# Kernel tuning notes

Hardware: AMD Instinct MI355X
Metric: run time of the kernel (lower is better)

The kernel has to match this reference:

```python
import jax, jax.numpy as jnp
import numpy as np

B, T, D, F, E, K = 4, 2048, 1024, 2048, 8, 2


def setup_inputs() -> dict:
    key = jax.random.key(0)
    ks = jax.random.split(key, 5)
    s = lambda n: 1.0 / np.sqrt(n)
    return {
        "x": jax.random.normal(ks[0], (B, T, D), jnp.float32),
        "gate_w": jax.random.normal(ks[1], (D, E), jnp.float32) * s(D),
        "gate_b": jnp.zeros((E,), jnp.float32),
        "w1": jax.random.normal(ks[2], (E, D, F), jnp.float32) * s(D),
        "b1": jnp.zeros((E, F), jnp.float32),
        "w2": jax.random.normal(ks[3], (E, F, D), jnp.float32) * s(F),
        "b2": jnp.zeros((E, D), jnp.float32),
    }


def reference(x, gate_w, gate_b, w1, b1, w2, b2):
    # Router: gate logits -> top-k -> softmax over the k selected logits
    logits = x @ gate_w + gate_b                      # [B,T,E]
    top_v, top_i = jax.lax.top_k(logits, K)           # [B,T,K]
    top_w = jax.nn.softmax(top_v, axis=-1)            # [B,T,K]
    # Dense combine weights per expert: w_full[b,t,e] = sum_k top_w * 1[top_i==e]
    one_hot = jax.nn.one_hot(top_i, E, dtype=x.dtype)  # [B,T,K,E]
    w_full = jnp.sum(top_w[..., None] * one_hot, axis=-2)  # [B,T,E]
    # All-experts FFN (batched over expert dim), exact-erf GELU as in nn.GELU()
    h = jax.nn.gelu(jnp.einsum('btd,edf->ebtf', x, w1) + b1[:, None, None, :],
                    approximate=False)                 # [E,B,T,F]
    y = jnp.einsum('ebtf,efd->ebtd', h, w2) + b2[:, None, None, :]  # [E,B,T,D]
    # Weighted combine (zero weight for unselected experts == masked dispatch)
    return jnp.einsum('bte,ebtd->btd', w_full, y)      # [B,T,D]
```

## Files before the change

kernel.cpp:

```cpp
#include <hip/hip_runtime.h>
#include <hip/hip_bf16.h>
#include <math.h>

#define B_ 4
#define T_ 2048
#define D_ 1024
#define F_ 2048
#define E_ 8
#define NT (B_ * T_)
#define NS (NT * 2)
#define CAP (NS + E_ * 256)

typedef __attribute__((ext_vector_type(8))) short short8;
typedef __attribute__((ext_vector_type(4))) float floatx4;

static __device__ __forceinline__ unsigned short f2bf(float f) {
  union { float f; unsigned u; } a; a.f = f;
  unsigned r = a.u + 0x7fffu + ((a.u >> 16) & 1u);
  return (unsigned short)(r >> 16);
}

static __device__ __forceinline__ float bf2f(unsigned u) {
  union { unsigned u; float f; } a; a.u = u << 16; return a.f;
}

static __device__ __forceinline__ void gld16(const unsigned short* g, unsigned short* l) {
  __builtin_amdgcn_global_load_lds(
      (const __attribute__((address_space(1))) void*)g,
      (__attribute__((address_space(3))) void*)l, 16, 0, 0);
}

static __device__ __forceinline__ float gelu_f(float v) {
  float ax = fabsf(v) * 0.70710678118654752f;
  float t = __builtin_amdgcn_rcpf(1.f + 0.3275911f * ax);
  float e = __builtin_amdgcn_exp2f(-ax * ax * 1.44269504088896f);
  float p = t * (0.254829592f +
            t * (-0.284496736f +
            t * (1.421413741f +
            t * (-1.453152027f +
            t * 1.061405429f))));
  float er = 1.f - p * e;
  er = copysignf(er, v);
  return 0.5f * v * (1.f + er);
}

__global__ void transpose_cvt(const float* __restrict__ in, unsigned short* __restrict__ out,
                              int R, int C) {
  __shared__ float tile[32][33];
  int e = blockIdx.z;
  const float* inp = in + (size_t)e * R * C;
  unsigned short* outp = out + (size_t)e * R * C;
  int c0 = blockIdx.x * 32, r0 = blockIdx.y * 32;
  int tx = threadIdx.x, ty = threadIdx.y;
#pragma unroll
  for (int j = 0; j < 4; j++)
    tile[ty + 8 * j][tx] = inp[(size_t)(r0 + ty + 8 * j) * C + c0 + tx];
  __syncthreads();
#pragma unroll
  for (int j = 0; j < 4; j++)
    outp[(size_t)(c0 + ty + 8 * j) * R + r0 + tx] = f2bf(tile[tx][ty + 8 * j]);
}

__global__ void router_k(const float* __restrict__ x, const float* __restrict__ gw,
                         const float* __restrict__ gb, int* __restrict__ ti,
                         float* __restrict__ tw) {
  int wid = threadIdx.x >> 6, lane = threadIdx.x & 63;
  int t = blockIdx.x * 4 + wid;
  const float* xr = x + (size_t)t * D_;
  float acc[E_];
#pragma unroll
  for (int e = 0; e < E_; e++) acc[e] = 0.f;
#pragma unroll
  for (int it = 0; it < D_ / 64; it++) {
    int d = it * 64 + lane;
    float xv = xr[d];
    const float* g = gw + d * E_;
#pragma unroll
    for (int e = 0; e < E_; e++) acc[e] += xv * g[e];
  }
#pragma unroll
  for (int off = 32; off > 0; off >>= 1)
#pragma unroll
    for (int e = 0; e < E_; e++) acc[e] += __shfl_xor(acc[e], off);
  if (lane == 0) {
    float v[E_];
#pragma unroll
    for (int e = 0; e < E_; e++) v[e] = acc[e] + gb[e];
    int i0 = 0; float v0 = v[0];
#pragma unroll
    for (int e = 1; e < E_; e++) if (v[e] > v0) { v0 = v[e]; i0 = e; }
    int i1 = -1; float v1 = -3.4e38f;
#pragma unroll
    for (int e = 0; e < E_; e++) if (e != i0 && v[e] > v1) { v1 = v[e]; i1 = e; }
    float ex = expf(v1 - v0);
    float w0 = 1.f / (1.f + ex);
    float w1 = ex / (1.f + ex);
    ti[2 * t] = i0; tw[2 * t] = w0;
    ti[2 * t + 1] = i1; tw[2 * t + 1] = w1;
  }
}

__global__ void count_prefix_k(const int* __restrict__ ti, int* __restrict__ offs,
                               int* __restrict__ cursors) {
  __shared__ int scnt[4][E_];
  int tid = threadIdx.x;
  int cnt[E_];
#pragma unroll
  for (int k = 0; k < E_; k++) cnt[k] = 0;
  for (int i = tid; i < NS; i += 256) {
    int e = ti[i];
#pragma unroll
    for (int k = 0; k < E_; k++) cnt[k] += (e == k) ? 1 : 0;
  }
#pragma unroll
  for (int off = 32; off > 0; off >>= 1)
#pragma unroll
    for (int k = 0; k < E_; k++) cnt[k] += __shfl_xor(cnt[k], off);
  int wid = tid >> 6, lane = tid & 63;
  if (lane == 0)
#pragma unroll
    for (int k = 0; k < E_; k++) scnt[wid][k] = cnt[k];
  __syncthreads();
  if (tid == 0) {
    int o = 0;
    for (int k = 0; k < E_; k++) {
      int c = scnt[0][k] + scnt[1][k] + scnt[2][k] + scnt[3][k];
      offs[k] = o;
      cursors[k] = o;
      o += (c + 255) & ~255;
    }
    offs[E_] = o;
  }
}

__global__ void fill_k(int* __restrict__ idx) {
  int s = blockIdx.x * 256 + threadIdx.x;
  if (s < CAP) idx[s] = 0;
}

__global__ void scatter_k(const int* __restrict__ ti, const float* __restrict__ tw,
                          int* __restrict__ cursors, int* __restrict__ idx,
                          int* __restrict__ pos_of) {
  int a = blockIdx.x * 256 + threadIdx.x;
  int lane = threadIdx.x & 63;
  int e = ti[a];
  unsigned long long m[E_];
#pragma unroll
  for (int k = 0; k < E_; k++) m[k] = __ballot(e == k);
  int base = 0;
  if (lane < E_) base = atomicAdd(&cursors[lane], __popcll(m[lane]));
  int myBase = __shfl(base, e);
  unsigned long long m_mine = 0;
#pragma unroll
  for (int k = 0; k < E_; k++) if (e == k) m_mine = m[k];
  int rank = __popcll(m_mine & ((1ull << lane) - 1ull));
  int pos = myBase + rank;
  idx[pos] = a >> 1;
  pos_of[a] = pos;
}

__global__ void gather_k(const float* __restrict__ x, const int* __restrict__ idx,
                         unsigned short* __restrict__ Xg) {
  int s = blockIdx.x;
  int t = idx[s];
  const float4* xr = (const float4*)(x + (size_t)t * D_);
  float4 v = xr[threadIdx.x];
  uint2 p;
  p.x = (unsigned)f2bf(v.x) | ((unsigned)f2bf(v.y) << 16);
  p.y = (unsigned)f2bf(v.z) | ((unsigned)f2bf(v.w) << 16);
  ((uint2*)(Xg + (size_t)s * D_))[threadIdx.x] = p;
}

template <int K, int N, bool GELU>
__global__ __launch_bounds__(512, 2) void gemm_k(const unsigned short* __restrict__ A,
                                                 const unsigned short* __restrict__ W,
                                                 const float* __restrict__ bias_all,
                                                 unsigned short* __restrict__ O,
                                                 const int* __restrict__ offs) {
  int slot0 = blockIdx.y * 256;
  if (slot0 >= offs[E_]) return;
  int e = 0;
  while (slot0 >= offs[e + 1]) e++;
  const unsigned short* Bp = W + (size_t)e * N * K;
  int n0 = blockIdx.x * 256;

  __shared__ unsigned short lA[2][256 * 64];
  __shared__ unsigned short lB[2][256 * 64];

  int tid = threadIdx.x;
  int wid = tid >> 6, lane = tid & 63;
  int wr = wid >> 2, wc = wid & 3;
  int quad = lane >> 4, l15 = lane & 15;
  int l7 = l15 & 7;

  int sr = lane >> 3;
  int ch = (lane & 7) ^ sr;
  const unsigned short* gA = A + (size_t)(slot0 + 8 * wid + sr) * K + ch * 8;
  const unsigned short* gB = Bp + (size_t)(n0 + 8 * wid + sr) * K + ch * 8;

#define STAGE_A(buf, q, kk) gld16(gA + (size_t)(q) * 64 * K + (size_t)(kk), \
                                  &lA[buf][((q) * 64 + 8 * wid) * 64])
#define STAGE_B(buf, q, kk) gld16(gB + (size_t)(q) * 64 * K + (size_t)(kk), \
                                  &lB[buf][((q) * 64 + 8 * wid) * 64])
#define SYNCV(n) asm volatile("s_waitcnt vmcnt(" #n ")\n\ts_barrier" ::: "memory")

#define PH(buf, mh, ks, ...) do {                                                   \
    short8 af_[4], bf_[4];                                                          \
    _Pragma("unroll")                                                               \
    for (int m_ = 0; m_ < 4; m_++) {                                                \
      int row_ = 128 * wr + 64 * (mh) + 16 * m_ + l15;                              \
      af_[m_] = *(const short8*)&lA[buf][row_ * 64 + ((((ks) << 2) | quad) ^ l7) * 8]; \
    }                                                                               \
    _Pragma("unroll")                                                               \
    for (int n_ = 0; n_ < 4; n_++) {                                                \
      int row_ = 64 * wc + 16 * n_ + l15;                                           \
      bf_[n_] = *(const short8*)&lB[buf][row_ * 64 + ((((ks) << 2) | quad) ^ l7) * 8]; \
    }                                                                               \
    __VA_ARGS__                                                                     \
    __builtin_amdgcn_sched_barrier(0x38F);                                          \
    __builtin_amdgcn_s_setprio(1);                                                  \
    _Pragma("unroll")                                                               \
    for (int m_ = 0; m_ < 4; m_++) {                                                \
      _Pragma("unroll")                                                             \
      for (int n_ = 0; n_ < 4; n_++)                                                \
        acc[4 * (mh) + m_][n_] = __builtin_amdgcn_mfma_f32_16x16x32_bf16(           \
            af_[m_], bf_[n_], acc[4 * (mh) + m_][n_], 0, 0, 0);                     \
    }                                                                               \
    __builtin_amdgcn_s_setprio(0);                                                  \
  } while (0)

  floatx4 acc[8][4];
#pragma unroll
  for (int mi = 0; mi < 8; mi++)
#pragma unroll
    for (int ni = 0; ni < 4; ni++) acc[mi][ni] = (floatx4){0.f, 0.f, 0.f, 0.f};

  STAGE_A(0, 0, 0); STAGE_A(0, 2, 0);
  STAGE_B(0, 0, 0); STAGE_B(0, 1, 0);
  STAGE_B(0, 2, 0); STAGE_B(0, 3, 0);
  __builtin_amdgcn_sched_barrier(0x38F);
  STAGE_A(0, 1, 0); STAGE_A(0, 3, 0);

  constexpr int NI = K / 128;
  for (int i = 0; i < NI; i++) {
    int kO = (2 * i + 1) * 64;
    int kE = (i + 1 < NI) ? (2 * i + 2) * 64 : 0;
    SYNCV(2);
    PH(0, 0, 0, STAGE_A(1, 0, kO); STAGE_A(1, 2, kO););
    PH(0, 0, 1, STAGE_B(1, 0, kO); STAGE_B(1, 1, kO););
    SYNCV(4);
    PH(0, 1, 0, STAGE_B(1, 2, kO); STAGE_B(1, 3, kO););
    PH(0, 1, 1, STAGE_A(1, 1, kO); STAGE_A(1, 3, kO););
    SYNCV(2);
    PH(1, 0, 0, STAGE_A(0, 0, kE); STAGE_A(0, 2, kE););
    PH(1, 0, 1, STAGE_B(0, 0, kE); STAGE_B(0, 1, kE););
    SYNCV(4);
    PH(1, 1, 0, STAGE_B(0, 2, kE); STAGE_B(0, 3, kE););
    PH(1, 1, 1, STAGE_A(0, 1, kE); STAGE_A(0, 3, kE););
  }

  const float* bias = bias_all + (size_t)e * N;
#pragma unroll
  for (int mi = 0; mi < 8; mi++) {
    int row = slot0 + 128 * wr + 16 * mi + quad * 4;
#pragma unroll
    for (int ni = 0; ni < 4; ni++) {
      int col = n0 + 64 * wc + 16 * ni + l15;
      float bv = bias[col];
#pragma unroll
      for (int r = 0; r < 4; r++) {
        float v = acc[mi][ni][r] + bv;
        if (GELU) v = gelu_f(v);
        O[(size_t)(row + r) * N + col] = f2bf(v);
      }
    }
  }
#undef STAGE_A
#undef STAGE_B
#undef SYNCV
#undef PH
}

__global__ void combine_k(const unsigned short* __restrict__ Yg,
                          const int* __restrict__ pos_of,
                          const float* __restrict__ tw, float* __restrict__ out) {
  int t = blockIdx.x;
  int p0 = pos_of[2 * t], p1 = pos_of[2 * t + 1];
  float w0 = tw[2 * t], w1 = tw[2 * t + 1];
  uint2 a = ((const uint2*)(Yg + (size_t)p0 * D_))[threadIdx.x];
  uint2 b = ((const uint2*)(Yg + (size_t)p1 * D_))[threadIdx.x];
  float4 r;
  r.x = w0 * bf2f(a.x & 0xffffu) + w1 * bf2f(b.x & 0xffffu);
  r.y = w0 * bf2f(a.x >> 16)     + w1 * bf2f(b.x >> 16);
  r.z = w0 * bf2f(a.y & 0xffffu) + w1 * bf2f(b.y & 0xffffu);
  r.w = w0 * bf2f(a.y >> 16)     + w1 * bf2f(b.y >> 16);
  ((float4*)(out + (size_t)t * D_))[threadIdx.x] = r;
}

extern "C" void kernel_launch(void* const* d_in, const int* in_sizes, int n_in,
                              void* d_out, int out_size, void* d_ws, size_t ws_size,
                              hipStream_t stream) {
  const float* x  = (const float*)d_in[0];
  const float* gw = (const float*)d_in[1];
  const float* gb = (const float*)d_in[2];
  const float* w1 = (const float*)d_in[3];
  const float* b1 = (const float*)d_in[4];
  const float* w2 = (const float*)d_in[5];
  const float* b2 = (const float*)d_in[6];
  float* out = (float*)d_out;

  char* p = (char*)d_ws;
  unsigned short* w1t = (unsigned short*)p; p += (size_t)E_ * D_ * F_ * 2;
  unsigned short* w2t = (unsigned short*)p; p += (size_t)E_ * D_ * F_ * 2;
  unsigned short* Xg  = (unsigned short*)p; p += (size_t)CAP * D_ * 2;
  unsigned short* H   = (unsigned short*)p; p += (size_t)CAP * F_ * 2;
  int*   idx    = (int*)p; p += (size_t)CAP * 4;
  int*   pos_of = (int*)p; p += (size_t)NS * 4;
  int*   ti     = (int*)p; p += (size_t)NS * 4;
  float* tw     = (float*)p; p += (size_t)NS * 4;
  int* cursors = (int*)p; p += 64;
  int* offs    = (int*)p; p += 64;
  unsigned short* Yg = Xg;

  dim3 tb(32, 8);
  transpose_cvt<<<dim3(F_ / 32, D_ / 32, E_), tb, 0, stream>>>(w1, w1t, D_, F_);
  transpose_cvt<<<dim3(D_ / 32, F_ / 32, E_), tb, 0, stream>>>(w2, w2t, F_, D_);
  router_k<<<NT / 4, 256, 0, stream>>>(x, gw, gb, ti, tw);
  count_prefix_k<<<1, 256, 0, stream>>>(ti, offs, cursors);
  fill_k<<<(CAP + 255) / 256, 256, 0, stream>>>(idx);
  scatter_k<<<NS / 256, 256, 0, stream>>>(ti, tw, cursors, idx, pos_of);
  gather_k<<<CAP, 256, 0, stream>>>(x, idx, Xg);
  gemm_k<D_, F_, true><<<dim3(F_ / 256, CAP / 256), 512, 0, stream>>>(Xg, w1t, b1, H, offs);
  gemm_k<F_, D_, false><<<dim3(D_ / 256, CAP / 256), 512, 0, stream>>>(H, w2t, b2, Yg, offs);
  combine_k<<<NT, 256, 0, stream>>>(Yg, pos_of, tw, out);
}
```

Measured before the change: 509.4 us.

## Rework MoE GEMM into 4-stage K=32 LDS pipeline and swap grid axes

Replaces the double-buffered K=64 LDS pipeline with a four-buffer ring of K=32 slices prefetched two steps ahead, using a new XOR swizzle for the fragment reads. Each step splits the MFMA work into two half-tiles with A and B staging interleaved between them. The grid axes are also swapped so blockIdx.x indexes token slots and blockIdx.y indexes output columns, which changes block dispatch order and L2 reuse of weights. The aim is deeper prefetch and better overlap of global loads with MFMA, at the cost of more barriers per K step.

```diff
diff --git a/kernel.cpp b/kernel.cpp
--- a/kernel.cpp
+++ b/kernel.cpp
@@ -177,56 +177,36 @@
                                                  const float* __restrict__ bias_all,
                                                  unsigned short* __restrict__ O,
                                                  const int* __restrict__ offs) {
-  int slot0 = blockIdx.y * 256;
+  int slot0 = blockIdx.x * 256;
   if (slot0 >= offs[E_]) return;
   int e = 0;
   while (slot0 >= offs[e + 1]) e++;
   const unsigned short* Bp = W + (size_t)e * N * K;
-  int n0 = blockIdx.x * 256;
-
-  __shared__ unsigned short lA[2][256 * 64];
-  __shared__ unsigned short lB[2][256 * 64];
+  int n0 = blockIdx.y * 256;
+
+  __shared__ unsigned short lA[4][256 * 32];
+  __shared__ unsigned short lB[4][256 * 32];
 
   int tid = threadIdx.x;
   int wid = tid >> 6, lane = tid & 63;
   int wr = wid >> 2, wc = wid & 3;
   int quad = lane >> 4, l15 = lane & 15;
-  int l7 = l15 & 7;
-
-  int sr = lane >> 3;
-  int ch = (lane & 7) ^ sr;
-  const unsigned short* gA = A + (size_t)(slot0 + 8 * wid + sr) * K + ch * 8;
-  const unsigned short* gB = Bp + (size_t)(n0 + 8 * wid + sr) * K + ch * 8;
-
-#define STAGE_A(buf, q, kk) gld16(gA + (size_t)(q) * 64 * K + (size_t)(kk), \
-                                  &lA[buf][((q) * 64 + 8 * wid) * 64])
-#define STAGE_B(buf, q, kk) gld16(gB + (size_t)(q) * 64 * K + (size_t)(kk), \
-                                  &lB[buf][((q) * 64 + 8 * wid) * 64])
-#define SYNCV(n) asm volatile("s_waitcnt vmcnt(" #n ")\n\ts_barrier" ::: "memory")
-
-#define PH(buf, mh, ks, ...) do {                                                   \
-    short8 af_[4], bf_[4];                                                          \
-    _Pragma("unroll")                                                               \
-    for (int m_ = 0; m_ < 4; m_++) {                                                \
-      int row_ = 128 * wr + 64 * (mh) + 16 * m_ + l15;                              \
-      af_[m_] = *(const short8*)&lA[buf][row_ * 64 + ((((ks) << 2) | quad) ^ l7) * 8]; \
-    }                                                                               \
-    _Pragma("unroll")                                                               \
-    for (int n_ = 0; n_ < 4; n_++) {                                                \
-      int row_ = 64 * wc + 16 * n_ + l15;                                           \
-      bf_[n_] = *(const short8*)&lB[buf][row_ * 64 + ((((ks) << 2) | quad) ^ l7) * 8]; \
-    }                                                                               \
-    __VA_ARGS__                                                                     \
-    __builtin_amdgcn_sched_barrier(0x38F);                                          \
-    __builtin_amdgcn_s_setprio(1);                                                  \
-    _Pragma("unroll")                                                               \
-    for (int m_ = 0; m_ < 4; m_++) {                                                \
-      _Pragma("unroll")                                                             \
-      for (int n_ = 0; n_ < 4; n_++)                                                \
-        acc[4 * (mh) + m_][n_] = __builtin_amdgcn_mfma_f32_16x16x32_bf16(           \
-            af_[m_], bf_[n_], acc[4 * (mh) + m_][n_], 0, 0, 0);                     \
-    }                                                                               \
-    __builtin_amdgcn_s_setprio(0);                                                  \
+
+  int cph = (((l15 & 1) << 2) | quad) ^ ((l15 >> 1) & 7);
+  int ra = ((wr << 6) + (l15 >> 1)) * 64 + cph * 8;
+  int rb = ((wc << 5) + (l15 >> 1)) * 64 + cph * 8;
+
+  int srl = lane >> 3;
+  int clog = (lane & 7) ^ srl;
+  int r_l = (srl << 1) | (clog >> 2);
+  int q_l = clog & 3;
+  const unsigned short* gA = A + (size_t)(slot0 + 16 * wid + r_l) * K + q_l * 8;
+  const unsigned short* gB = Bp + (size_t)(n0 + 16 * wid + r_l) * K + q_l * 8;
+
+#define STG(gp, larr, buf, kt) do {                                             \
+    gld16(gp + (size_t)(kt) * 32, &larr[buf][(16 * wid) * 32]);                 \
+    gld16(gp + (size_t)128 * K + (size_t)(kt) * 32,                             \
+          &larr[buf][(16 * wid + 128) * 32]);                                   \
   } while (0)
 
   floatx4 acc[8][4];
@@ -235,29 +215,44 @@
 #pragma unroll
     for (int ni = 0; ni < 4; ni++) acc[mi][ni] = (floatx4){0.f, 0.f, 0.f, 0.f};
 
-  STAGE_A(0, 0, 0); STAGE_A(0, 2, 0);
-  STAGE_B(0, 0, 0); STAGE_B(0, 1, 0);
-  STAGE_B(0, 2, 0); STAGE_B(0, 3, 0);
-  __builtin_amdgcn_sched_barrier(0x38F);
-  STAGE_A(0, 1, 0); STAGE_A(0, 3, 0);
-
-  constexpr int NI = K / 128;
-  for (int i = 0; i < NI; i++) {
-    int kO = (2 * i + 1) * 64;
-    int kE = (i + 1 < NI) ? (2 * i + 2) * 64 : 0;
-    SYNCV(2);
-    PH(0, 0, 0, STAGE_A(1, 0, kO); STAGE_A(1, 2, kO););
-    PH(0, 0, 1, STAGE_B(1, 0, kO); STAGE_B(1, 1, kO););
-    SYNCV(4);
-    PH(0, 1, 0, STAGE_B(1, 2, kO); STAGE_B(1, 3, kO););
-    PH(0, 1, 1, STAGE_A(1, 1, kO); STAGE_A(1, 3, kO););
-    SYNCV(2);
-    PH(1, 0, 0, STAGE_A(0, 0, kE); STAGE_A(0, 2, kE););
-    PH(1, 0, 1, STAGE_B(0, 0, kE); STAGE_B(0, 1, kE););
-    SYNCV(4);
-    PH(1, 1, 0, STAGE_B(0, 2, kE); STAGE_B(0, 3, kE););
-    PH(1, 1, 1, STAGE_A(0, 1, kE); STAGE_A(0, 3, kE););
-  }
+  STG(gA, lA, 0, 0); STG(gB, lB, 0, 0);
+  STG(gA, lA, 1, 1); STG(gB, lB, 1, 1);
+  asm volatile("s_waitcnt vmcnt(4)\ns_barrier" ::: "memory");
+
+  constexpr int NK = K / 32;
+  for (int t = 0; t < NK; t++) {
+    int buf = t & 3, sb = (t + 2) & 3;
+    int kt = (t + 2 < NK) ? (t + 2) : 0;
+    short8 af[4], bfr[4];
+#pragma unroll
+    for (int m = 0; m < 4; m++) af[m] = *(const short8*)&lA[buf][ra + m * 512];
+#pragma unroll
+    for (int n = 0; n < 4; n++) bfr[n] = *(const short8*)&lB[buf][rb + n * 512];
+    STG(gA, lA, sb, kt);
+    asm volatile("s_barrier" ::: "memory");
+    __builtin_amdgcn_s_setprio(1);
+#pragma unroll
+    for (int m = 0; m < 4; m++)
+#pragma unroll
+      for (int n = 0; n < 4; n++)
+        acc[m][n] = __builtin_amdgcn_mfma_f32_16x16x32_bf16(af[m], bfr[n], acc[m][n], 0, 0, 0);
+    __builtin_amdgcn_s_setprio(0);
+    asm volatile("s_barrier" ::: "memory");
+    short8 ag[4];
+#pragma unroll
+    for (int m = 0; m < 4; m++) ag[m] = *(const short8*)&lA[buf][ra + (m + 4) * 512];
+    STG(gB, lB, sb, kt);
+    asm volatile("s_barrier" ::: "memory");
+    __builtin_amdgcn_s_setprio(1);
+#pragma unroll
+    for (int m = 0; m < 4; m++)
+#pragma unroll
+      for (int n = 0; n < 4; n++)
+        acc[m + 4][n] = __builtin_amdgcn_mfma_f32_16x16x32_bf16(ag[m], bfr[n], acc[m + 4][n], 0, 0, 0);
+    __builtin_amdgcn_s_setprio(0);
+    asm volatile("s_waitcnt vmcnt(4)\ns_barrier" ::: "memory");
+  }
+#undef STG
 
   const float* bias = bias_all + (size_t)e * N;
 #pragma unroll
@@ -275,10 +270,6 @@
       }
     }
   }
-#undef STAGE_A
-#undef STAGE_B
-#undef SYNCV
-#undef PH
 }
 
 __global__ void combine_k(const unsigned short* __restrict__ Yg,
@@ -330,7 +321,7 @@
   fill_k<<<(CAP + 255) / 256, 256, 0, stream>>>(idx);
   scatter_k<<<NS / 256, 256, 0, stream>>>(ti, tw, cursors, idx, pos_of);
   gather_k<<<CAP, 256, 0, stream>>>(x, idx, Xg);
-  gemm_k<D_, F_, true><<<dim3(F_ / 256, CAP / 256), 512, 0, stream>>>(Xg, w1t, b1, H, offs);
-  gemm_k<F_, D_, false><<<dim3(D_ / 256, CAP / 256), 512, 0, stream>>>(H, w2t, b2, Yg, offs);
+  gemm_k<D_, F_, true><<<dim3(CAP / 256, F_ / 256), 512, 0, stream>>>(Xg, w1t, b1, H, offs);
+  gemm_k<F_, D_, false><<<dim3(CAP / 256, D_ / 256), 512, 0, stream>>>(H, w2t, b2, Yg, offs);
   combine_k<<<NT, 256, 0, stream>>>(Yg, pos_of, tw, out);
 }
```

Result: faster. 496.7 us (-2.5%).
